# Performance work log

Measured on AMD Instinct MI355X. Metric: run time of the kernel, lower is better.

Reference implementation:

```python
import jax, jax.numpy as jnp
import numpy as np

NUM_EXPERTS = 8

def setup_inputs() -> dict:
    key = jax.random.key(0)
    k1, k2, k3, k4, k5 = jax.random.split(key, 5)
    T, D, H, O, E, K = 4096, 1024, 2048, 1024, NUM_EXPERTS, 2
    hidden_states = jax.random.normal(k1, (T, D), dtype=jnp.float32)
    top_k_indices = jax.random.randint(k2, (T, K), 0, E, dtype=jnp.int64)
    top_k_weights = jax.random.uniform(k3, (T, K), dtype=jnp.float32)
    gate_up_proj = jax.random.normal(k4, (E, 2 * H, D), dtype=jnp.float32) * 0.02
    down_proj = jax.random.normal(k5, (E, O, H), dtype=jnp.float32) * 0.02
    return {
        "hidden_states": hidden_states,
        "top_k_indices": top_k_indices,
        "top_k_weights": top_k_weights,
        "gate_up_proj": gate_up_proj,
        "down_proj": down_proj,
    }


def _moe(hidden_states, top_k_weights, gate_up_proj, down_proj, top_k_indices):
    # Mathematically identical to the torch per-token-gather loop, expressed as
    # dense all-expert compute + sparse combine (non-selected experts get weight 0).
    T = hidden_states.shape[0]
    E = gate_up_proj.shape[0]
    # [T, E, 2H]
    gate_up = jnp.einsum('td,ehd->teh', hidden_states, gate_up_proj)
    gate, up = jnp.split(gate_up, 2, axis=-1)
    h = jax.nn.silu(gate) * up  # [T, E, H]
    expert_out = jnp.einsum('teh,eoh->teo', h, down_proj)  # [T, E, O]
    # combine weights: scatter top-k routing weights into [T, E]
    combine = jnp.zeros((T, E), dtype=hidden_states.dtype)
    rows = jnp.arange(T)[:, None]
    combine = combine.at[rows, top_k_indices].add(top_k_weights)
    return jnp.einsum('teo,te->to', expert_out, combine)


def reference(hidden_states, top_k_indices, top_k_weights, gate_up_proj, down_proj):
    return _moe(hidden_states, top_k_weights, gate_up_proj, down_proj, top_k_indices)
```

## Files before the change

kernel.cpp:

```cpp
#include <hip/hip_runtime.h>
#include <stdint.h>

#define TOKS 4096
#define DIM  1024
#define HID  2048
#define OUTD 1024
#define NE   8
#define MP   9216
#define NBR  72

typedef __bf16 bf16;
typedef bf16 bf16x8 __attribute__((ext_vector_type(8)));
typedef float f32x4 __attribute__((ext_vector_type(4)));
typedef __attribute__((address_space(1))) void gvoid;
typedef __attribute__((address_space(3))) void lvoid;

#define WGU_OFF  0ull
#define WD_OFF   (WGU_OFF + 67108864ull)
#define XG_OFF   (WD_OFF  + 33554432ull)
#define H_OFF    (XG_OFF  + 18874368ull)
#define TK_OFF   (H_OFF   + 37748736ull)
#define SW_OFF   (TK_OFF  + 36864ull)
#define META_OFF (SW_OFF  + 36864ull)
#define T2S_OFF  (META_OFF + 1024ull)

__device__ __forceinline__ unsigned short f2bf(float f) {
  union { float f; unsigned u; } v; v.f = f;
  unsigned r = (v.u + 0x7FFFu + ((v.u >> 16) & 1u)) >> 16;
  return (unsigned short)r;
}
__device__ __forceinline__ unsigned pack2(float a, float b) {
  return (unsigned)f2bf(a) | ((unsigned)f2bf(b) << 16);
}
__device__ __forceinline__ void cp16(const void* g, void* l) {
  __builtin_amdgcn_global_load_lds((gvoid*)(void*)g, (lvoid*)l, 16, 0, 0);
}

__global__ void init_kernel(int* __restrict__ slot_token, int* __restrict__ counts) {
  int gid = blockIdx.x * 256 + threadIdx.x;
  if (gid < MP) slot_token[gid] = -1;
  if (gid < NE) counts[gid] = 0;
}

__global__ void count_kernel(const int* __restrict__ idx, int* __restrict__ counts) {
  int gid = blockIdx.x * 256 + threadIdx.x;
  int lane = threadIdx.x & 63;
  int e = (gid < TOKS * 2) ? idx[gid] : -1;
#pragma unroll
  for (int ex = 0; ex < NE; ++ex) {
    unsigned long long mask = __ballot(e == ex);
    if (lane == 0 && mask) atomicAdd(&counts[ex], __popcll(mask));
  }
}

__global__ void offsets_kernel(int* __restrict__ meta) {
  if (threadIdx.x != 0) return;
  int* counts = meta; int* offs = meta + 8; int* cursors = meta + 16; int* table = meta + 24;
  int cum = 0;
  for (int e = 0; e < NE; ++e) {
    offs[e] = cum; cursors[e] = 0;
    int nb = (counts[e] + 127) >> 7;
    int bb = cum >> 7;
    for (int b = 0; b < nb; ++b) table[bb + b] = e;
    cum += nb << 7;
  }
  for (int b = cum >> 7; b < NBR; ++b) table[b] = -1;
}

__global__ void scatter_kernel(const int* __restrict__ idx, const float* __restrict__ wts,
                               int* __restrict__ meta, int* __restrict__ slot_token,
                               float* __restrict__ slot_w, int* __restrict__ tok2slot) {
  int gid = blockIdx.x * 256 + threadIdx.x;
  int lane = threadIdx.x & 63;
  int e = (gid < TOKS * 2) ? idx[gid] : -1;
  int pos = -1;
#pragma unroll
  for (int ex = 0; ex < NE; ++ex) {
    unsigned long long mask = __ballot(e == ex);
    if (e == ex) {
      int rank = __popcll(mask & ((1ull << lane) - 1ull));
      int leader = __ffsll(mask) - 1;
      int base = 0;
      if (lane == leader) base = atomicAdd(&meta[16 + ex], __popcll(mask));
      base = __shfl(base, leader);
      pos = meta[8 + ex] + base + rank;
    }
  }
  if (e >= 0) {
    slot_token[pos] = gid >> 1;
    slot_w[pos] = wts[gid];
    tok2slot[gid] = pos;
  }
}

__global__ void gather_kernel(const float* __restrict__ X, const int* __restrict__ slot_token,
                              uint4* __restrict__ Xg) {
  int gid = blockIdx.x * 256 + threadIdx.x;
  int row = gid >> 7, j = (gid & 127) << 3;
  int t = slot_token[row];
  uint4 o;
  if (t >= 0) {
    const float4* p = (const float4*)(X + (size_t)t * DIM + j);
    float4 a = p[0], b = p[1];
    o.x = pack2(a.x, a.y); o.y = pack2(a.z, a.w);
    o.z = pack2(b.x, b.y); o.w = pack2(b.z, b.w);
  } else {
    o = uint4{0u, 0u, 0u, 0u};
  }
  Xg[gid] = o;
}

__global__ void convert_kernel(const float4* __restrict__ src, uint2* __restrict__ dst, int n4) {
  int i = blockIdx.x * 256 + threadIdx.x;
  if (i >= n4) return;
  float4 v = src[i];
  uint2 o; o.x = pack2(v.x, v.y); o.y = pack2(v.z, v.w);
  dst[i] = o;
}

__global__ void combine_kernel(const float* __restrict__ Obuf, const int* __restrict__ tok2slot,
                               const float* __restrict__ slot_w, float4* __restrict__ out) {
  int t = blockIdx.x, c = threadIdx.x;
  int s0 = tok2slot[2 * t], s1 = tok2slot[2 * t + 1];
  float w0 = slot_w[s0], w1 = slot_w[s1];
  float4 a = ((const float4*)(Obuf + (size_t)s0 * OUTD))[c];
  float4 b = ((const float4*)(Obuf + (size_t)s1 * OUTD))[c];
  out[(size_t)t * (OUTD / 4) + c] =
      float4{w0 * a.x + w1 * b.x, w0 * a.y + w1 * b.y, w0 * a.z + w1 * b.z, w0 * a.w + w1 * b.w};
}

__global__ __launch_bounds__(256) void gemm1_kernel(
    const unsigned short* __restrict__ Xg,
    const unsigned short* __restrict__ Wgu,
    unsigned short* __restrict__ Hbuf,
    const int* __restrict__ table) {
  int e = table[blockIdx.y];
  if (e < 0) return;
  const int tid = threadIdx.x;
  const int lane = tid & 63, wave = tid >> 6;
  const int wm = wave >> 1, wn = wave & 1;
  const int lr = lane & 15, quad = lane >> 4;

  __shared__ bf16 As[128 * 32];
  __shared__ bf16 Bg[64 * 32];
  __shared__ bf16 Bu[64 * 32];

  const unsigned short* A_base  = Xg  + (size_t)blockIdx.y * 128 * DIM;
  const unsigned short* Wg_base = Wgu + (size_t)e * 2 * HID * DIM + (size_t)(blockIdx.x * 64) * DIM;
  const unsigned short* Wu_base = Wg_base + (size_t)HID * DIM;

  const int srow = tid >> 2;
  const int sldc = (tid & 3) * 8;
  const int sgc  = ((tid & 3) ^ ((srow >> 1) & 3)) * 8;
  const int cq = (quad ^ ((lr >> 1) & 3)) * 8;

  f32x4 accg[4][2] = {}; f32x4 accu[4][2] = {};

  for (int kt = 0; kt < DIM / 32; ++kt) {
    const int kb = kt * 32;
    cp16(A_base  + (size_t)srow * DIM + kb + sgc,        (void*)(As + srow * 32 + sldc));
    cp16(A_base  + (size_t)(srow + 64) * DIM + kb + sgc, (void*)(As + (srow + 64) * 32 + sldc));
    cp16(Wg_base + (size_t)srow * DIM + kb + sgc,        (void*)(Bg + srow * 32 + sldc));
    cp16(Wu_base + (size_t)srow * DIM + kb + sgc,        (void*)(Bu + srow * 32 + sldc));
    __syncthreads();
    bf16x8 a[4], bg[2], bu[2];
#pragma unroll
    for (int i = 0; i < 4; ++i)
      a[i] = *(const bf16x8*)(As + (wm * 64 + i * 16 + lr) * 32 + cq);
#pragma unroll
    for (int j = 0; j < 2; ++j) {
      bg[j] = *(const bf16x8*)(Bg + (wn * 32 + j * 16 + lr) * 32 + cq);
      bu[j] = *(const bf16x8*)(Bu + (wn * 32 + j * 16 + lr) * 32 + cq);
    }
#pragma unroll
    for (int i = 0; i < 4; ++i)
#pragma unroll
      for (int j = 0; j < 2; ++j) {
        accg[i][j] = __builtin_amdgcn_mfma_f32_16x16x32_bf16(a[i], bg[j], accg[i][j], 0, 0, 0);
        accu[i][j] = __builtin_amdgcn_mfma_f32_16x16x32_bf16(a[i], bu[j], accu[i][j], 0, 0, 0);
      }
    __syncthreads();
  }

  const int rowBase = blockIdx.y * 128 + wm * 64;
  const int colBase = blockIdx.x * 64 + wn * 32;
#pragma unroll
  for (int i = 0; i < 4; ++i)
#pragma unroll
    for (int r = 0; r < 4; ++r) {
      int row = rowBase + i * 16 + quad * 4 + r;
#pragma unroll
      for (int j = 0; j < 2; ++j) {
        float g = accg[i][j][r], u = accu[i][j][r];
        float s = g / (1.0f + __expf(-g));
        Hbuf[(size_t)row * HID + colBase + j * 16 + lr] = f2bf(s * u);
      }
    }
}

__global__ __launch_bounds__(256) void gemm2_kernel(
    const unsigned short* __restrict__ Hbuf,
    const unsigned short* __restrict__ Wd,
    float* __restrict__ Obuf,
    const int* __restrict__ table) {
  int e = table[blockIdx.y];
  if (e < 0) return;
  const int tid = threadIdx.x;
  const int lane = tid & 63, wave = tid >> 6;
  const int wm = wave >> 1, wn = wave & 1;
  const int lr = lane & 15, quad = lane >> 4;

  __shared__ bf16 As[128 * 32];
  __shared__ bf16 Bs[128 * 32];

  const unsigned short* A_base = Hbuf + (size_t)blockIdx.y * 128 * HID;
  const unsigned short* B_base = Wd + (size_t)e * OUTD * HID + (size_t)(blockIdx.x * 128) * HID;

  const int srow = tid >> 2;
  const int sldc = (tid & 3) * 8;
  const int sgc  = ((tid & 3) ^ ((srow >> 1) & 3)) * 8;
  const int cq = (quad ^ ((lr >> 1) & 3)) * 8;

  f32x4 acc[4][4] = {};

  for (int kt = 0; kt < HID / 32; ++kt) {
    const int kb = kt * 32;
    cp16(A_base + (size_t)srow * HID + kb + sgc,        (void*)(As + srow * 32 + sldc));
    cp16(A_base + (size_t)(srow + 64) * HID + kb + sgc, (void*)(As + (srow + 64) * 32 + sldc));
    cp16(B_base + (size_t)srow * HID + kb + sgc,        (void*)(Bs + srow * 32 + sldc));
    cp16(B_base + (size_t)(srow + 64) * HID + kb + sgc, (void*)(Bs + (srow + 64) * 32 + sldc));
    __syncthreads();
    bf16x8 a[4], b[4];
#pragma unroll
    for (int i = 0; i < 4; ++i)
      a[i] = *(const bf16x8*)(As + (wm * 64 + i * 16 + lr) * 32 + cq);
#pragma unroll
    for (int j = 0; j < 4; ++j)
      b[j] = *(const bf16x8*)(Bs + (wn * 64 + j * 16 + lr) * 32 + cq);
#pragma unroll
    for (int i = 0; i < 4; ++i)
#pragma unroll
      for (int j = 0; j < 4; ++j)
        acc[i][j] = __builtin_amdgcn_mfma_f32_16x16x32_bf16(a[i], b[j], acc[i][j], 0, 0, 0);
    __syncthreads();
  }

  const int rowBase = blockIdx.y * 128 + wm * 64;
  const int colBase = blockIdx.x * 128 + wn * 64;
#pragma unroll
  for (int i = 0; i < 4; ++i)
#pragma unroll
    for (int r = 0; r < 4; ++r) {
      int row = rowBase + i * 16 + quad * 4 + r;
      float* Orow = Obuf + (size_t)row * OUTD + colBase;
#pragma unroll
      for (int j = 0; j < 4; ++j)
        Orow[j * 16 + lr] = acc[i][j][r];
    }
}

extern "C" void kernel_launch(void* const* d_in, const int* in_sizes, int n_in,
                              void* d_out, int out_size, void* d_ws, size_t ws_size,
                              hipStream_t stream) {
  const float* X     = (const float*)d_in[0];
  const int*   idx   = (const int*)d_in[1];
  const float* wts   = (const float*)d_in[2];
  const float* WguF  = (const float*)d_in[3];
  const float* WdF   = (const float*)d_in[4];
  float* out = (float*)d_out;

  char* base = (char*)d_ws;
  unsigned short* Wgu = (unsigned short*)(base + WGU_OFF);
  unsigned short* Wd  = (unsigned short*)(base + WD_OFF);
  unsigned short* Xg  = (unsigned short*)(base + XG_OFF);
  unsigned short* Hb  = (unsigned short*)(base + H_OFF);
  float* Obuf         = (float*)(base + WGU_OFF);
  int*   slot_token = (int*)(base + TK_OFF);
  float* slot_w     = (float*)(base + SW_OFF);
  int*   meta       = (int*)(base + META_OFF);
  int*   table      = meta + 24;
  int*   tok2slot   = (int*)(base + T2S_OFF);

  init_kernel<<<MP / 256, 256, 0, stream>>>(slot_token, meta);
  count_kernel<<<(TOKS * 2) / 256, 256, 0, stream>>>(idx, meta);
  offsets_kernel<<<1, 64, 0, stream>>>(meta);
  scatter_kernel<<<(TOKS * 2) / 256, 256, 0, stream>>>(idx, wts, meta, slot_token, slot_w, tok2slot);
  gather_kernel<<<(MP * 128) / 256, 256, 0, stream>>>(X, slot_token, (uint4*)Xg);
  convert_kernel<<<(NE * 2 * HID * DIM / 4) / 256, 256, 0, stream>>>(
      (const float4*)WguF, (uint2*)Wgu, NE * 2 * HID * DIM / 4);
  convert_kernel<<<(NE * OUTD * HID / 4) / 256, 256, 0, stream>>>(
      (const float4*)WdF, (uint2*)Wd, NE * OUTD * HID / 4);
  gemm1_kernel<<<dim3(HID / 64, NBR), 256, 0, stream>>>(Xg, Wgu, Hb, table);
  gemm2_kernel<<<dim3(OUTD / 128, NBR), 256, 0, stream>>>(Hb, Wd, Obuf, table);
  combine_kernel<<<TOKS, 256, 0, stream>>>(Obuf, tok2slot, slot_w, (float4*)out);
}
```

Before: 493.4 us.

## Merge routing kernels, fuse weight conversion, and double GEMM K-tile to 64

The four routing kernels (init, count, offsets, scatter) are replaced by a single one-block route kernel that uses shared-memory counters. The two weight-conversion launches are merged into one. The combine step now reads routing weights directly, which removes the slot_w buffer. Both GEMMs now load 64-wide K tiles with an 8-way XOR swizzle and run two MFMA sub-steps per barrier, halving the number of syncs; this doubles LDS per block and may reduce occupancy.

```diff
diff --git a/kernel.cpp b/kernel.cpp
--- a/kernel.cpp
+++ b/kernel.cpp
@@ -20,8 +20,7 @@
 #define XG_OFF   (WD_OFF  + 33554432ull)
 #define H_OFF    (XG_OFF  + 18874368ull)
 #define TK_OFF   (H_OFF   + 37748736ull)
-#define SW_OFF   (TK_OFF  + 36864ull)
-#define META_OFF (SW_OFF  + 36864ull)
+#define META_OFF (TK_OFF  + 36864ull)
 #define T2S_OFF  (META_OFF + 1024ull)
 
 __device__ __forceinline__ unsigned short f2bf(float f) {
@@ -36,60 +35,58 @@
   __builtin_amdgcn_global_load_lds((gvoid*)(void*)g, (lvoid*)l, 16, 0, 0);
 }
 
-__global__ void init_kernel(int* __restrict__ slot_token, int* __restrict__ counts) {
-  int gid = blockIdx.x * 256 + threadIdx.x;
-  if (gid < MP) slot_token[gid] = -1;
-  if (gid < NE) counts[gid] = 0;
-}
-
-__global__ void count_kernel(const int* __restrict__ idx, int* __restrict__ counts) {
-  int gid = blockIdx.x * 256 + threadIdx.x;
-  int lane = threadIdx.x & 63;
-  int e = (gid < TOKS * 2) ? idx[gid] : -1;
-#pragma unroll
-  for (int ex = 0; ex < NE; ++ex) {
-    unsigned long long mask = __ballot(e == ex);
-    if (lane == 0 && mask) atomicAdd(&counts[ex], __popcll(mask));
-  }
-}
-
-__global__ void offsets_kernel(int* __restrict__ meta) {
-  if (threadIdx.x != 0) return;
-  int* counts = meta; int* offs = meta + 8; int* cursors = meta + 16; int* table = meta + 24;
-  int cum = 0;
-  for (int e = 0; e < NE; ++e) {
-    offs[e] = cum; cursors[e] = 0;
-    int nb = (counts[e] + 127) >> 7;
-    int bb = cum >> 7;
-    for (int b = 0; b < nb; ++b) table[bb + b] = e;
-    cum += nb << 7;
-  }
-  for (int b = cum >> 7; b < NBR; ++b) table[b] = -1;
-}
-
-__global__ void scatter_kernel(const int* __restrict__ idx, const float* __restrict__ wts,
-                               int* __restrict__ meta, int* __restrict__ slot_token,
-                               float* __restrict__ slot_w, int* __restrict__ tok2slot) {
-  int gid = blockIdx.x * 256 + threadIdx.x;
-  int lane = threadIdx.x & 63;
-  int e = (gid < TOKS * 2) ? idx[gid] : -1;
-  int pos = -1;
-#pragma unroll
-  for (int ex = 0; ex < NE; ++ex) {
-    unsigned long long mask = __ballot(e == ex);
-    if (e == ex) {
-      int rank = __popcll(mask & ((1ull << lane) - 1ull));
-      int leader = __ffsll(mask) - 1;
-      int base = 0;
-      if (lane == leader) base = atomicAdd(&meta[16 + ex], __popcll(mask));
-      base = __shfl(base, leader);
-      pos = meta[8 + ex] + base + rank;
-    }
-  }
-  if (e >= 0) {
-    slot_token[pos] = gid >> 1;
-    slot_w[pos] = wts[gid];
-    tok2slot[gid] = pos;
+__global__ __launch_bounds__(1024) void route_kernel(const int* __restrict__ idx,
+                                                     int* __restrict__ table,
+                                                     int* __restrict__ slot_token,
+                                                     int* __restrict__ tok2slot) {
+  __shared__ int cnt[NE], offs[NE], cur[NE];
+  const int tid = threadIdx.x, lane = tid & 63;
+  for (int i = tid; i < MP; i += 1024) slot_token[i] = -1;
+  if (tid < NE) cnt[tid] = 0;
+  __syncthreads();
+  int myE[8];
+#pragma unroll
+  for (int c = 0; c < 8; ++c) myE[c] = idx[c * 1024 + tid];
+#pragma unroll
+  for (int c = 0; c < 8; ++c) {
+    int e = myE[c];
+#pragma unroll
+    for (int ex = 0; ex < NE; ++ex) {
+      unsigned long long m = __ballot(e == ex);
+      if (lane == 0 && m) atomicAdd(&cnt[ex], __popcll(m));
+    }
+  }
+  __syncthreads();
+  if (tid == 0) {
+    int cum = 0;
+    for (int e = 0; e < NE; ++e) {
+      offs[e] = cum; cur[e] = 0;
+      int nb = (cnt[e] + 127) >> 7;
+      int bb = cum >> 7;
+      for (int b = 0; b < nb; ++b) table[bb + b] = e;
+      cum += nb << 7;
+    }
+    for (int b = cum >> 7; b < NBR; ++b) table[b] = -1;
+  }
+  __syncthreads();
+#pragma unroll
+  for (int c = 0; c < 8; ++c) {
+    int e = myE[c];
+    int pos = 0;
+#pragma unroll
+    for (int ex = 0; ex < NE; ++ex) {
+      unsigned long long m = __ballot(e == ex);
+      if (e == ex) {
+        int rank = __popcll(m & ((1ull << lane) - 1ull));
+        int leader = __ffsll(m) - 1;
+        int base = 0;
+        if (lane == leader) base = atomicAdd(&cur[ex], __popcll(m));
+        base = __shfl(base, leader);
+        pos = offs[ex] + base + rank;
+      }
+    }
+    slot_token[pos] = (c * 1024 + tid) >> 1;
+    tok2slot[c * 1024 + tid] = pos;
   }
 }
 
@@ -110,19 +107,22 @@
   Xg[gid] = o;
 }
 
-__global__ void convert_kernel(const float4* __restrict__ src, uint2* __restrict__ dst, int n4) {
+__global__ void convert_kernel(const float4* __restrict__ srcGu, uint2* __restrict__ dstGu,
+                               const float4* __restrict__ srcD, uint2* __restrict__ dstD) {
+  const int n1 = NE * 2 * HID * DIM / 4;
   int i = blockIdx.x * 256 + threadIdx.x;
-  if (i >= n4) return;
-  float4 v = src[i];
+  float4 v; uint2* dp;
+  if (i < n1) { v = srcGu[i]; dp = dstGu + i; }
+  else        { v = srcD[i - n1]; dp = dstD + (i - n1); }
   uint2 o; o.x = pack2(v.x, v.y); o.y = pack2(v.z, v.w);
-  dst[i] = o;
+  *dp = o;
 }
 
 __global__ void combine_kernel(const float* __restrict__ Obuf, const int* __restrict__ tok2slot,
-                               const float* __restrict__ slot_w, float4* __restrict__ out) {
+                               const float* __restrict__ wts, float4* __restrict__ out) {
   int t = blockIdx.x, c = threadIdx.x;
   int s0 = tok2slot[2 * t], s1 = tok2slot[2 * t + 1];
-  float w0 = slot_w[s0], w1 = slot_w[s1];
+  float w0 = wts[2 * t], w1 = wts[2 * t + 1];
   float4 a = ((const float4*)(Obuf + (size_t)s0 * OUTD))[c];
   float4 b = ((const float4*)(Obuf + (size_t)s1 * OUTD))[c];
   out[(size_t)t * (OUTD / 4) + c] =
@@ -141,44 +141,54 @@
   const int wm = wave >> 1, wn = wave & 1;
   const int lr = lane & 15, quad = lane >> 4;
 
-  __shared__ bf16 As[128 * 32];
-  __shared__ bf16 Bg[64 * 32];
-  __shared__ bf16 Bu[64 * 32];
+  __shared__ bf16 As[128 * 64];
+  __shared__ bf16 Bg[64 * 64];
+  __shared__ bf16 Bu[64 * 64];
 
   const unsigned short* A_base  = Xg  + (size_t)blockIdx.y * 128 * DIM;
   const unsigned short* Wg_base = Wgu + (size_t)e * 2 * HID * DIM + (size_t)(blockIdx.x * 64) * DIM;
   const unsigned short* Wu_base = Wg_base + (size_t)HID * DIM;
 
-  const int srow = tid >> 2;
-  const int sldc = (tid & 3) * 8;
-  const int sgc  = ((tid & 3) ^ ((srow >> 1) & 3)) * 8;
-  const int cq = (quad ^ ((lr >> 1) & 3)) * 8;
-
   f32x4 accg[4][2] = {}; f32x4 accu[4][2] = {};
 
-  for (int kt = 0; kt < DIM / 32; ++kt) {
-    const int kb = kt * 32;
-    cp16(A_base  + (size_t)srow * DIM + kb + sgc,        (void*)(As + srow * 32 + sldc));
-    cp16(A_base  + (size_t)(srow + 64) * DIM + kb + sgc, (void*)(As + (srow + 64) * 32 + sldc));
-    cp16(Wg_base + (size_t)srow * DIM + kb + sgc,        (void*)(Bg + srow * 32 + sldc));
-    cp16(Wu_base + (size_t)srow * DIM + kb + sgc,        (void*)(Bu + srow * 32 + sldc));
+  for (int kt = 0; kt < DIM / 64; ++kt) {
+    const int kb = kt * 64;
+#pragma unroll
+    for (int i = 0; i < 4; ++i) {
+      int s = i * 256 + tid, row = s >> 3, pc = s & 7, gc = pc ^ (row & 7);
+      cp16(A_base + (size_t)row * DIM + kb + gc * 8, (void*)(As + row * 64 + pc * 8));
+    }
+#pragma unroll
+    for (int i = 0; i < 2; ++i) {
+      int s = i * 256 + tid, row = s >> 3, pc = s & 7, gc = pc ^ (row & 7);
+      cp16(Wg_base + (size_t)row * DIM + kb + gc * 8, (void*)(Bg + row * 64 + pc * 8));
+      cp16(Wu_base + (size_t)row * DIM + kb + gc * 8, (void*)(Bu + row * 64 + pc * 8));
+    }
     __syncthreads();
-    bf16x8 a[4], bg[2], bu[2];
-#pragma unroll
-    for (int i = 0; i < 4; ++i)
-      a[i] = *(const bf16x8*)(As + (wm * 64 + i * 16 + lr) * 32 + cq);
-#pragma unroll
-    for (int j = 0; j < 2; ++j) {
-      bg[j] = *(const bf16x8*)(Bg + (wn * 32 + j * 16 + lr) * 32 + cq);
-      bu[j] = *(const bf16x8*)(Bu + (wn * 32 + j * 16 + lr) * 32 + cq);
-    }
-#pragma unroll
-    for (int i = 0; i < 4; ++i)
+#pragma unroll
+    for (int ks = 0; ks < 2; ++ks) {
+      bf16x8 a[4], bg[2], bu[2];
+#pragma unroll
+      for (int i = 0; i < 4; ++i) {
+        int row = wm * 64 + i * 16 + lr;
+        int pc = (ks * 4 + quad) ^ (row & 7);
+        a[i] = *(const bf16x8*)(As + row * 64 + pc * 8);
+      }
 #pragma unroll
       for (int j = 0; j < 2; ++j) {
-        accg[i][j] = __builtin_amdgcn_mfma_f32_16x16x32_bf16(a[i], bg[j], accg[i][j], 0, 0, 0);
-        accu[i][j] = __builtin_amdgcn_mfma_f32_16x16x32_bf16(a[i], bu[j], accu[i][j], 0, 0, 0);
-      }
+        int row = wn * 32 + j * 16 + lr;
+        int pc = (ks * 4 + quad) ^ (row & 7);
+        bg[j] = *(const bf16x8*)(Bg + row * 64 + pc * 8);
+        bu[j] = *(const bf16x8*)(Bu + row * 64 + pc * 8);
+      }
+#pragma unroll
+      for (int i = 0; i < 4; ++i)
+#pragma unroll
+        for (int j = 0; j < 2; ++j) {
+          accg[i][j] = __builtin_amdgcn_mfma_f32_16x16x32_bf16(a[i], bg[j], accg[i][j], 0, 0, 0);
+          accu[i][j] = __builtin_amdgcn_mfma_f32_16x16x32_bf16(a[i], bu[j], accu[i][j], 0, 0, 0);
+        }
+    }
     __syncthreads();
   }
 
@@ -210,38 +220,44 @@
   const int wm = wave >> 1, wn = wave & 1;
   const int lr = lane & 15, quad = lane >> 4;
 
-  __shared__ bf16 As[128 * 32];
-  __shared__ bf16 Bs[128 * 32];
+  __shared__ bf16 As[128 * 64];
+  __shared__ bf16 Bs[128 * 64];
 
   const unsigned short* A_base = Hbuf + (size_t)blockIdx.y * 128 * HID;
   const unsigned short* B_base = Wd + (size_t)e * OUTD * HID + (size_t)(blockIdx.x * 128) * HID;
 
-  const int srow = tid >> 2;
-  const int sldc = (tid & 3) * 8;
-  const int sgc  = ((tid & 3) ^ ((srow >> 1) & 3)) * 8;
-  const int cq = (quad ^ ((lr >> 1) & 3)) * 8;
-
   f32x4 acc[4][4] = {};
 
-  for (int kt = 0; kt < HID / 32; ++kt) {
-    const int kb = kt * 32;
-    cp16(A_base + (size_t)srow * HID + kb + sgc,        (void*)(As + srow * 32 + sldc));
-    cp16(A_base + (size_t)(srow + 64) * HID + kb + sgc, (void*)(As + (srow + 64) * 32 + sldc));
-    cp16(B_base + (size_t)srow * HID + kb + sgc,        (void*)(Bs + srow * 32 + sldc));
-    cp16(B_base + (size_t)(srow + 64) * HID + kb + sgc, (void*)(Bs + (srow + 64) * 32 + sldc));
+  for (int kt = 0; kt < HID / 64; ++kt) {
+    const int kb = kt * 64;
+#pragma unroll
+    for (int i = 0; i < 4; ++i) {
+      int s = i * 256 + tid, row = s >> 3, pc = s & 7, gc = pc ^ (row & 7);
+      cp16(A_base + (size_t)row * HID + kb + gc * 8, (void*)(As + row * 64 + pc * 8));
+      cp16(B_base + (size_t)row * HID + kb + gc * 8, (void*)(Bs + row * 64 + pc * 8));
+    }
     __syncthreads();
-    bf16x8 a[4], b[4];
-#pragma unroll
-    for (int i = 0; i < 4; ++i)
-      a[i] = *(const bf16x8*)(As + (wm * 64 + i * 16 + lr) * 32 + cq);
-#pragma unroll
-    for (int j = 0; j < 4; ++j)
-      b[j] = *(const bf16x8*)(Bs + (wn * 64 + j * 16 + lr) * 32 + cq);
-#pragma unroll
-    for (int i = 0; i < 4; ++i)
-#pragma unroll
-      for (int j = 0; j < 4; ++j)
-        acc[i][j] = __builtin_amdgcn_mfma_f32_16x16x32_bf16(a[i], b[j], acc[i][j], 0, 0, 0);
+#pragma unroll
+    for (int ks = 0; ks < 2; ++ks) {
+      bf16x8 a[4], b[4];
+#pragma unroll
+      for (int i = 0; i < 4; ++i) {
+        int row = wm * 64 + i * 16 + lr;
+        int pc = (ks * 4 + quad) ^ (row & 7);
+        a[i] = *(const bf16x8*)(As + row * 64 + pc * 8);
+      }
+#pragma unroll
+      for (int j = 0; j < 4; ++j) {
+        int row = wn * 64 + j * 16 + lr;
+        int pc = (ks * 4 + quad) ^ (row & 7);
+        b[j] = *(const bf16x8*)(Bs + row * 64 + pc * 8);
+      }
+#pragma unroll
+      for (int i = 0; i < 4; ++i)
+#pragma unroll
+        for (int j = 0; j < 4; ++j)
+          acc[i][j] = __builtin_amdgcn_mfma_f32_16x16x32_bf16(a[i], b[j], acc[i][j], 0, 0, 0);
+    }
     __syncthreads();
   }
 
@@ -276,21 +292,17 @@
   unsigned short* Hb  = (unsigned short*)(base + H_OFF);
   float* Obuf         = (float*)(base + WGU_OFF);
   int*   slot_token = (int*)(base + TK_OFF);
-  float* slot_w     = (float*)(base + SW_OFF);
-  int*   meta       = (int*)(base + META_OFF);
-  int*   table      = meta + 24;
+  int*   table      = (int*)(base + META_OFF);
   int*   tok2slot   = (int*)(base + T2S_OFF);
 
-  init_kernel<<<MP / 256, 256, 0, stream>>>(slot_token, meta);
-  count_kernel<<<(TOKS * 2) / 256, 256, 0, stream>>>(idx, meta);
-  offsets_kernel<<<1, 64, 0, stream>>>(meta);
-  scatter_kernel<<<(TOKS * 2) / 256, 256, 0, stream>>>(idx, wts, meta, slot_token, slot_w, tok2slot);
+  route_kernel<<<1, 1024, 0, stream>>>(idx, table, slot_token, tok2slot);
   gather_kernel<<<(MP * 128) / 256, 256, 0, stream>>>(X, slot_token, (uint4*)Xg);
-  convert_kernel<<<(NE * 2 * HID * DIM / 4) / 256, 256, 0, stream>>>(
-      (const float4*)WguF, (uint2*)Wgu, NE * 2 * HID * DIM / 4);
-  convert_kernel<<<(NE * OUTD * HID / 4) / 256, 256, 0, stream>>>(
-      (const float4*)WdF, (uint2*)Wd, NE * OUTD * HID / 4);
+  {
+    const int nTot = (NE * 2 * HID * DIM + NE * OUTD * HID) / 4;
+    convert_kernel<<<nTot / 256, 256, 0, stream>>>((const float4*)WguF, (uint2*)Wgu,
+                                                   (const float4*)WdF, (uint2*)Wd);
+  }
   gemm1_kernel<<<dim3(HID / 64, NBR), 256, 0, stream>>>(Xg, Wgu, Hb, table);
   gemm2_kernel<<<dim3(OUTD / 128, NBR), 256, 0, stream>>>(Hb, Wd, Obuf, table);
-  combine_kernel<<<TOKS, 256, 0, stream>>>(Obuf, tok2slot, slot_w, (float4*)out);
-}
+  combine_kernel<<<TOKS, 256, 0, stream>>>(Obuf, tok2slot, wts, (float4*)out);
+}
```

New measurement: 438.6 us. 1.12x faster.
